# Kernel tuning notes

Hardware: AMD Instinct MI355X
Metric: run time of the kernel (lower is better)

Reference implementation:

```python
import jax, jax.numpy as jnp
import numpy as np
from functools import partial

MAX_SPAN_WIDTH = 8


def setup_inputs() -> dict:
    key = jax.random.key(0)
    ks = jax.random.split(key, 8)
    B, S, H = 4, 256, 256
    NE, D = 50000, 256  # entity_embedding_dim == hidden_size
    inp = {
        "embeddings": jax.random.normal(ks[0], (B, S, H), jnp.float32),          # BERT outputs[0]
        "entity_table": jax.random.normal(ks[1], (NE, D), jnp.float32) * 0.02,   # nn.Embedding weight
        "span_W": jax.random.normal(ks[2], (2 * H + 1, H), jnp.float32) * 0.02,  # span_embedding Linear
        "span_b": jax.random.normal(ks[3], (H,), jnp.float32) * 0.02,
        "gcn_W1": jax.random.normal(ks[4], (D, H), jnp.float32) * 0.02,
        "gcn_b1": jax.random.normal(ks[5], (H,), jnp.float32) * 0.02,
        "gcn_W2": jax.random.normal(ks[6], (H, H), jnp.float32) * 0.02,
        "gcn_b2": jax.random.normal(ks[7], (H,), jnp.float32) * 0.02,
        "k": 8,
    }
    return inp


def _star_adj_norm(k, dtype):
    # k-node star graph (node 0 hub) with self-loops, symmetric GCN normalization
    A = jnp.zeros((k, k), dtype).at[0, 1:].set(1.0).at[1:, 0].set(1.0) + jnp.eye(k, dtype=dtype)
    deg = A.sum(axis=1)
    return A / jnp.sqrt(deg[:, None] * deg[None, :])


def reference(embeddings, entity_table, span_W, span_b, gcn_W1, gcn_b1, gcn_W2, gcn_b2, k):
    B, S, H = embeddings.shape
    Wmax = MAX_SPAN_WIDTH
    dtype = embeddings.dtype

    # token_inputs: CLS embedding per example
    cls = embeddings[:, 0, :]  # [B, H]

    # Vectorized ragged span max-pool: running max over widths 1..Wmax.
    # span_max[w, b, s, :] = max(embeddings[b, s : s+w+1, :])
    neg_inf = jnp.array(-jnp.inf, dtype)
    maxes = []
    cur = embeddings
    maxes.append(cur)
    for w in range(1, Wmax):
        shifted = jnp.concatenate(
            [embeddings[:, w:, :], jnp.full((B, w, H), neg_inf, dtype)], axis=1)
        cur = jnp.maximum(cur, shifted)  # -inf pad => out-of-range positions ignored
        maxes.append(cur)
    span_max = jnp.stack(maxes, axis=0)  # [Wmax, B, S, H]

    # concat(max-pool, CLS, span width) -> span_embedding Linear
    cls_b = jnp.broadcast_to(cls[None, :, None, :], (Wmax, B, S, H))
    width_feat = jnp.broadcast_to(
        jnp.arange(1, Wmax + 1, dtype=dtype)[:, None, None, None], (Wmax, B, S, 1))
    span_inputs = jnp.concatenate([span_max, cls_b, width_feat], axis=-1)  # [Wmax,B,S,2H+1]
    span_inputs = span_inputs.reshape(Wmax * B * S, 2 * H + 1)             # [N, 2H+1]
    span_repr = span_inputs @ span_W + span_b                              # [N, H]

    # build_subgraph: top-k similar entities per span (memory-bound similarity + top-k)
    sims = span_repr @ entity_table.T          # [N, NE]  ~1.6GB intermediate
    _, topk_idx = jax.lax.top_k(sims, k)       # [N, k]
    node_x = entity_table[topk_idx]            # gather -> [N, k, D]

    # 2-layer GCN on the fixed star subgraph (gather-linear-scatter equivalent)
    A_norm = _star_adj_norm(k, dtype)          # [k, k]
    h = jax.nn.relu(jnp.einsum('ij,njd,dh->nih', A_norm, node_x, gcn_W1) + gcn_b1)
    subgraph_out = jnp.einsum('ij,njd,dh->nih', A_norm, h, gcn_W2) + gcn_b2  # [N, k, H]

    return cls, span_repr, subgraph_out
```

## Files before the change

kernel.cpp:

```cpp
#include <hip/hip_runtime.h>

typedef unsigned short u16;
typedef unsigned int   u32;
typedef unsigned long long u64;
typedef short bf16x8 __attribute__((ext_vector_type(8)));
typedef float f32x4  __attribute__((ext_vector_type(4)));

#define INF_F __builtin_inff()

__device__ __forceinline__ u16 f2bf(float f) {
  u32 u = __float_as_uint(f);
  return (u16)((u + 0x7FFFu + ((u >> 16) & 1u)) >> 16);
}

__device__ __forceinline__ u32 sortf(float f) {
  u32 u = __float_as_uint(f);
  return u ^ ((u32)((int)u >> 31) | 0x80000000u);
}
__device__ __forceinline__ float unsortf(u32 s) {
  u32 u = s ^ ((s & 0x80000000u) ? 0x80000000u : 0xFFFFFFFFu);
  return __uint_as_float(u);
}
__device__ __forceinline__ u64 sx64(u64 v, int m) {
  u32 lo = __shfl_xor((u32)v, m);
  u32 hi = __shfl_xor((u32)(v >> 32), m);
  return ((u64)hi << 32) | lo;
}

__device__ __forceinline__ void gload_lds16(const void* g, void* l) {
  __builtin_amdgcn_global_load_lds(
      (const __attribute__((address_space(1))) u32*)g,
      (__attribute__((address_space(3))) u32*)l, 16, 0, 0);
}

__global__ __launch_bounds__(256) void k0_cvt(
    const float* __restrict__ src, u16* __restrict__ dst, int n4) {
  int id = blockIdx.x * 256 + threadIdx.x;
  if (id >= n4) return;
  float4 v = ((const float4*)src)[id];
  ((ushort4*)dst)[id] = make_ushort4(f2bf(v.x), f2bf(v.y), f2bf(v.z), f2bf(v.w));
}

__global__ __launch_bounds__(256) void k1_span(
    const float* __restrict__ emb, const float* __restrict__ Wsp,
    const float* __restrict__ bsp,
    float* __restrict__ out0, float* __restrict__ out1,
    u16* __restrict__ spanbf) {
  __shared__ float SM[8][256];
  __shared__ float CLS[256];
  const int bid = blockIdx.x;
  const int b = bid >> 8, s = bid & 255;
  const int t = threadIdx.x;
  const float* eb = emb + (size_t)b * 65536;

  CLS[t] = eb[t];
  if (s == 0) out0[b * 256 + t] = eb[t];

  float m = eb[s * 256 + t];
  SM[0][t] = m;
  #pragma unroll
  for (int w = 1; w < 8; ++w) {
    if (s + w < 256) m = fmaxf(m, eb[(s + w) * 256 + t]);
    SM[w][t] = m;
  }
  __syncthreads();

  float cc = 0.f;
  for (int k = 0; k < 256; k += 4) {
    float4 cq = *(const float4*)&CLS[k];
    cc += cq.x * Wsp[(size_t)(256 + k + 0) * 256 + t];
    cc += cq.y * Wsp[(size_t)(256 + k + 1) * 256 + t];
    cc += cq.z * Wsp[(size_t)(256 + k + 2) * 256 + t];
    cc += cq.w * Wsp[(size_t)(256 + k + 3) * 256 + t];
  }
  float acc[8];
  const float base = bsp[t] + cc;
  #pragma unroll
  for (int w = 0; w < 8; ++w) acc[w] = base;

  for (int k = 0; k < 256; k += 4) {
    float w0 = Wsp[(size_t)(k + 0) * 256 + t];
    float w1 = Wsp[(size_t)(k + 1) * 256 + t];
    float w2 = Wsp[(size_t)(k + 2) * 256 + t];
    float w3 = Wsp[(size_t)(k + 3) * 256 + t];
    #pragma unroll
    for (int w = 0; w < 8; ++w) {
      float4 smq = *(const float4*)&SM[w][k];
      acc[w] += smq.x * w0; acc[w] += smq.y * w1;
      acc[w] += smq.z * w2; acc[w] += smq.w * w3;
    }
  }
  const float wm = Wsp[(size_t)512 * 256 + t];
  #pragma unroll
  for (int w = 0; w < 8; ++w) {
    float val = acc[w] + (float)(w + 1) * wm;
    size_t idx = ((size_t)w * 1024 + bid) * 256 + t;
    out1[idx] = val;
    spanbf[idx] = f2bf(val);
  }
}

__global__ __launch_bounds__(128, 4) void k2_mfma(
    const u16* __restrict__ spanbf, const u16* __restrict__ entbf, int ne,
    float* __restrict__ Rpv, int* __restrict__ Rpi) {
  __shared__ u32 Elds[4096];
  __shared__ u64 Q[2][32][8];
  const int t = threadIdx.x, lane = t & 63, wv = t >> 6;
  const int m = lane & 15, q = lane >> 4, q4 = q * 4;
  const int p = blockIdx.x & 15, rg = blockIdx.x >> 4;
  const int psz = (ne + 15) >> 4;
  const int e_start = p * psz;
  const int e_end = min(ne, e_start + psz);
  const int rowbase = rg * 64 + wv * 32;
  const u64 gm = 0xFFFFull << (q * 16);
  const u64 lanelow = (lane == 63) ? 0x7FFFFFFFFFFFFFFFull
                                   : ((1ull << (lane + 1)) - 1) >> 1;
  const u64 gml = gm & lanelow;
  const int row = lane & 15;
  const int ls5 = lane >> 5;

  const u64 KINIT = ((u64)sortf(-INF_F) << 32);
  u64 slot[2][4];
  float myth[2], th[2][4];
  #pragma unroll
  for (int h = 0; h < 2; ++h) {
    myth[h] = -INF_F;
    #pragma unroll
    for (int s = 0; s < 4; ++s) { slot[h][s] = KINIT; th[h][s] = -INF_F; }
  }

  bf16x8 a[2][8];
  #pragma unroll
  for (int h = 0; h < 2; ++h)
    #pragma unroll
    for (int s = 0; s < 8; ++s)
      a[h][s] = *(const bf16x8*)(spanbf
                  + (size_t)(rowbase + h * 16 + m) * 256 + s * 32 + q * 8);

  auto issue = [&](int k, int sl) {
    const int cb = e_start + (k << 4);
    #pragma unroll
    for (int i = 0; i < 4; ++i) {
      int eo = wv * 8 + i * 2 + ls5;
      int e  = (sl << 4) + eo;
      int ge = min(cb + eo, e_end - 1);
      int xoff = ((lane & 31) ^ (e & 31)) << 4;
      gload_lds16((const char*)entbf + (size_t)ge * 512 + xoff,
                  (char*)Elds + (sl << 13) + (wv << 12) + (i << 10));
    }
  };

  const int nch = (e_end - e_start + 15) >> 4;
  issue(0, 0);

  for (int pc = 0; pc < nch; ++pc) {
    const int cs = pc & 1;
    asm volatile("s_waitcnt vmcnt(0)" ::: "memory");
    __builtin_amdgcn_sched_barrier(0);
    __builtin_amdgcn_s_barrier();
    if (pc + 1 < nch) issue(pc + 1, cs ^ 1);

    f32x4 acc[2];
    #pragma unroll
    for (int h = 0; h < 2; ++h) acc[h] = (f32x4){0.f, 0.f, 0.f, 0.f};
    const int el = (cs << 4) + m, sw = el & 31, bc = el << 5;
    #pragma unroll
    for (int s = 0; s < 8; ++s) {
      int qq = s * 4 + q;
      bf16x8 bfr = *(const bf16x8*)((const char*)Elds + ((bc | (qq ^ sw)) << 4));
      #pragma unroll
      for (int h = 0; h < 2; ++h)
        acc[h] = __builtin_amdgcn_mfma_f32_16x16x32_bf16(a[h][s], bfr, acc[h], 0, 0, 0);
    }
    const int gent = e_start + (pc << 4) + m;
    const bool valid = gent < e_end;

    #pragma unroll
    for (int h = 0; h < 2; ++h) {
      bool any = valid & ((acc[h][0] > th[h][0]) | (acc[h][1] > th[h][1]) |
                          (acc[h][2] > th[h][2]) | (acc[h][3] > th[h][3]));
      if (!__ballot(any)) continue;
      u64 M[4]; u64 key[4]; int ps_[4]; bool hit[4];
      #pragma unroll
      for (int r = 0; r < 4; ++r) {
        hit[r] = valid && (acc[h][r] > th[h][r]);
        M[r] = __ballot(hit[r]);
        key[r] = ((u64)sortf(acc[h][r]) << 32) | (u32)(~(u32)gent);
        ps_[r] = (int)__popcll(M[r] & gml);
        if (hit[r] && ps_[r] < 8)
          Q[wv][h * 16 + q4 + r][(ps_[r] ^ (q4 + r)) & 7] = key[r];
      }
      u64 msk = (row & 2) ? ((row & 1) ? M[3] : M[2])
                          : ((row & 1) ? M[1] : M[0]);
      int cnt = (int)__popcll((msk >> ((row >> 2) << 4)) & 0xFFFFull);
      int cmax = cnt;
      #pragma unroll
      for (int o = 1; o < 16; o <<= 1)
        cmax = max(cmax, __shfl_xor(cmax, o));
      const u64* qrow = Q[wv][h * 16 + row];
      const int rx = row & 7;
      int cm1 = min(cmax, 8);
      for (int j = 0; j < cm1; ++j) {
        u64 cand = (j < cnt) ? qrow[(j ^ rx) & 7] : 0;
        u64 m01 = slot[h][0] < slot[h][1] ? slot[h][0] : slot[h][1];
        u64 m23 = slot[h][2] < slot[h][3] ? slot[h][2] : slot[h][3];
        u64 lmin = m01 < m23 ? m01 : m23;
        u64 g = sx64(lmin, 16); if (g < lmin) lmin = g;
        g = sx64(lmin, 32); u64 gmin = (g < lmin) ? g : lmin;
        bool ins = cand > gmin;
        #pragma unroll
        for (int s2 = 0; s2 < 4; ++s2)
          if (ins && slot[h][s2] == gmin) slot[h][s2] = cand;
      }
      if (cmax > 8) {
        #pragma unroll
        for (int r = 0; r < 4; ++r)
          if (hit[r] && ps_[r] >= 8)
            Q[wv][h * 16 + q4 + r][((ps_[r] - 8) ^ (q4 + r)) & 7] = key[r];
        for (int j = 8; j < cmax; ++j) {
          u64 cand = (j < cnt) ? qrow[((j - 8) ^ rx) & 7] : 0;
          u64 m01 = slot[h][0] < slot[h][1] ? slot[h][0] : slot[h][1];
          u64 m23 = slot[h][2] < slot[h][3] ? slot[h][2] : slot[h][3];
          u64 lmin = m01 < m23 ? m01 : m23;
          u64 g = sx64(lmin, 16); if (g < lmin) lmin = g;
          g = sx64(lmin, 32); u64 gmin = (g < lmin) ? g : lmin;
          bool ins = cand > gmin;
          #pragma unroll
          for (int s2 = 0; s2 < 4; ++s2)
            if (ins && slot[h][s2] == gmin) slot[h][s2] = cand;
        }
      }
      {
        u64 m01 = slot[h][0] < slot[h][1] ? slot[h][0] : slot[h][1];
        u64 m23 = slot[h][2] < slot[h][3] ? slot[h][2] : slot[h][3];
        u64 lmin = m01 < m23 ? m01 : m23;
        u64 g = sx64(lmin, 16); if (g < lmin) lmin = g;
        g = sx64(lmin, 32); if (g < lmin) lmin = g;
        myth[h] = unsortf((u32)(lmin >> 32));
        #pragma unroll
        for (int r = 0; r < 4; ++r) th[h][r] = __shfl(myth[h], q4 + r);
      }
    }
  }

  {
    const int sg = lane >> 4;
    #pragma unroll
    for (int h = 0; h < 2; ++h) {
      int r0 = rowbase + h * 16 + row;
      #pragma unroll
      for (int s = 0; s < 4; ++s) {
        u64 e0 = slot[h][s];
        int col = p * 16 + sg * 4 + s;
        Rpv[(size_t)r0 * 256 + col] = unsortf((u32)(e0 >> 32));
        Rpi[(size_t)r0 * 256 + col] = (int)(~(u32)e0);
      }
    }
  }
}

__global__ __launch_bounds__(256) void k2_merge(
    const float* __restrict__ Rpv, const int* __restrict__ Rpi,
    int* __restrict__ Ridx) {
  const int t = threadIdx.x, lane = t & 63, wv = t >> 6;
  const int row = blockIdx.x * 4 + wv;
  float v[4]; int e[4];
  #pragma unroll
  for (int pg = 0; pg < 4; ++pg) {
    v[pg] = Rpv[(size_t)row * 256 + pg * 64 + lane];
    e[pg] = Rpi[(size_t)row * 256 + pg * 64 + lane];
  }
  int c[4] = {0, 0, 0, 0};
  #pragma unroll
  for (int ps = 0; ps < 4; ++ps) {
    for (int i = 0; i < 64; ++i) {
      float ov = __shfl(v[ps], i); int oi = __shfl(e[ps], i);
      #pragma unroll
      for (int pd = 0; pd < 4; ++pd)
        c[pd] += (ov > v[pd] || (ov == v[pd] && oi < e[pd]));
    }
  }
  #pragma unroll
  for (int pg = 0; pg < 4; ++pg)
    if (c[pg] < 16) Ridx[(size_t)row * 16 + c[pg]] = e[pg];
}

__global__ __launch_bounds__(256, 3) void k3_gcn(
    const float* __restrict__ out1, const float* __restrict__ ent,
    const int* __restrict__ Ridx,
    const float* __restrict__ W1, const float* __restrict__ b1,
    const float* __restrict__ W2, const float* __restrict__ b2,
    float* __restrict__ out2, int ne) {
  __shared__ __align__(16) char UN[34560];
  __shared__ __align__(16) u16 Abf[32][272];
  __shared__ int cidx[4][16];
  __shared__ int chos[4][8];
  const int t = threadIdx.x;
  const int lane = t & 63, wv = t >> 6;
  const int m = lane & 15, q = lane >> 4;
  const int n0 = blockIdx.x * 4;

  {
    float  (*SPR)[256] = (float (*)[256])UN;
    double (*dpart)[4] = (double (*)[4])(UN + 4096);
    double (*sims)[16] = (double (*)[16])(UN + 6144);
    #pragma unroll
    for (int g = 0; g < 4; ++g)
      SPR[g][t] = out1[(size_t)(n0 + g) * 256 + t];
    if (t < 64) {
      int g = t >> 4, j = t & 15;
      int c = Ridx[(size_t)(n0 + g) * 16 + j];
      if ((unsigned)c >= (unsigned)ne) c = 0;
      cidx[g][j] = c;
    }
    __syncthreads();

    {
      const int pr = t >> 2, sub = t & 3;
      const int g = pr >> 4, j = pr & 15;
      const float* er = ent + (size_t)cidx[g][j] * 256 + sub * 64;
      const float* sr = &SPR[g][sub * 64];
      double s = 0.0;
      #pragma unroll
      for (int i = 0; i < 64; i += 4) {
        float4 e4 = *(const float4*)&er[i];
        float4 s4 = *(const float4*)&sr[i];
        s += (double)e4.x * (double)s4.x;
        s += (double)e4.y * (double)s4.y;
        s += (double)e4.z * (double)s4.z;
        s += (double)e4.w * (double)s4.w;
      }
      dpart[pr][sub] = s;
    }
    __syncthreads();
    if (t < 64) {
      int g = t >> 4, j = t & 15;
      sims[g][j] = dpart[t][0] + dpart[t][1] + dpart[t][2] + dpart[t][3];
    }
    __syncthreads();
    if (t < 4) {
      unsigned used = 0;
      for (int o = 0; o < 8; ++o) {
        int best = -1; double bv = 0.0; int bi = 0;
        for (int j = 0; j < 16; ++j) {
          if (used & (1u << j)) continue;
          if (best < 0 || sims[t][j] > bv || (sims[t][j] == bv && cidx[t][j] < bi)) {
            best = j; bv = sims[t][j]; bi = cidx[t][j];
          }
        }
        used |= (1u << best);
        chos[t][o] = cidx[t][best];
      }
    }
    __syncthreads();
  }

  {
    const int r = t >> 3, cb = t & 7;
    const float* src = ent + (size_t)chos[r >> 3][r & 7] * 256 + cb * 32;
    u32 pk[16];
    #pragma unroll
    for (int i = 0; i < 8; ++i) {
      float4 v = *(const float4*)&src[i * 4];
      pk[2 * i]     = (u32)f2bf(v.x) | ((u32)f2bf(v.y) << 16);
      pk[2 * i + 1] = (u32)f2bf(v.z) | ((u32)f2bf(v.w) << 16);
    }
    uint4* dst = (uint4*)&Abf[r][cb * 32];
    #pragma unroll
    for (int i = 0; i < 4; ++i)
      dst[i] = make_uint4(pk[4 * i], pk[4 * i + 1], pk[4 * i + 2], pk[4 * i + 3]);
  }

  auto run_gemm = [&](const float* __restrict__ Wg) {
    f32x4 acc[2][4];
    #pragma unroll
    for (int mt = 0; mt < 2; ++mt)
      #pragma unroll
      for (int nt = 0; nt < 4; ++nt)
        acc[mt][nt] = (f32x4){0.f, 0.f, 0.f, 0.f};

    for (int s = 0; s < 8; ++s) {
      __syncthreads();
      {
        const float* src = Wg + (size_t)(s * 32) * 256 + t;
        u32 pk[16];
        #pragma unroll
        for (int i = 0; i < 16; ++i) {
          float lo = src[(size_t)(2 * i) * 256];
          float hi = src[(size_t)(2 * i + 1) * 256];
          pk[i] = (u32)f2bf(lo) | ((u32)f2bf(hi) << 16);
        }
        uint4* dst = (uint4*)(UN + t * 80);
        #pragma unroll
        for (int i = 0; i < 4; ++i)
          dst[i] = make_uint4(pk[4 * i], pk[4 * i + 1], pk[4 * i + 2], pk[4 * i + 3]);
      }
      __syncthreads();
      #pragma unroll
      for (int mt = 0; mt < 2; ++mt) {
        bf16x8 af = *(const bf16x8*)((const char*)Abf
                       + (mt * 16 + m) * 544 + s * 64 + q * 16);
        #pragma unroll
        for (int nt = 0; nt < 4; ++nt) {
          const int col = wv * 64 + nt * 16 + m;
          bf16x8 bf = *(const bf16x8*)(UN + col * 80 + q * 16);
          acc[mt][nt] = __builtin_amdgcn_mfma_f32_16x16x32_bf16(
              af, bf, acc[mt][nt], 0, 0, 0);
        }
      }
    }
    __syncthreads();
    #pragma unroll
    for (int mt = 0; mt < 2; ++mt)
      #pragma unroll
      for (int nt = 0; nt < 4; ++nt)
        #pragma unroll
        for (int r = 0; r < 4; ++r)
          *(float*)(UN + (((mt * 16 + q * 4 + r) * 268)
                          + (wv * 64 + nt * 16 + m)) * 4) = acc[mt][nt][r];
    __syncthreads();
  };

  run_gemm(W1);
  {
    const float bb = b1[t];
    #pragma unroll
    for (int g = 0; g < 4; ++g) {
      float v[8];
      #pragma unroll
      for (int j = 0; j < 8; ++j)
        v[j] = *(const float*)(UN + ((g * 8 + j) * 268 + t) * 4);
      float ssum = 0.f;
      #pragma unroll
      for (int j = 1; j < 8; ++j) ssum += v[j];
      Abf[g * 8][t] = f2bf(fmaxf(v[0] * 0.125f + ssum * 0.25f + bb, 0.f));
      #pragma unroll
      for (int j = 1; j < 8; ++j)
        Abf[g * 8 + j][t] = f2bf(fmaxf(v[0] * 0.25f + v[j] * 0.5f + bb, 0.f));
    }
  }

  run_gemm(W2);
  {
    const float bb = b2[t];
    #pragma unroll
    for (int g = 0; g < 4; ++g) {
      float v[8];
      #pragma unroll
      for (int j = 0; j < 8; ++j)
        v[j] = *(const float*)(UN + ((g * 8 + j) * 268 + t) * 4);
      float ssum = 0.f;
      #pragma unroll
      for (int j = 1; j < 8; ++j) ssum += v[j];
      float* ob = out2 + (size_t)(n0 + g) * 2048 + t;
      ob[0] = v[0] * 0.125f + ssum * 0.25f + bb;
      #pragma unroll
      for (int j = 1; j < 8; ++j)
        ob[(size_t)j * 256] = v[0] * 0.25f + v[j] * 0.5f + bb;
    }
  }
}

extern "C" void kernel_launch(void* const* d_in, const int* in_sizes, int n_in,
                              void* d_out, int out_size, void* d_ws, size_t ws_size,
                              hipStream_t stream) {
  const float* emb = (const float*)d_in[0];
  const float* ent = (const float*)d_in[1];
  const float* Wsp = (const float*)d_in[2];
  const float* bsp = (const float*)d_in[3];
  const float* W1  = (const float*)d_in[4];
  const float* b1  = (const float*)d_in[5];
  const float* W2  = (const float*)d_in[6];
  const float* b2  = (const float*)d_in[7];
  const int ne = in_sizes[1] / 256;

  float* out  = (float*)d_out;
  float* out0 = out;
  float* out1 = out + 1024;
  float* out2 = out + 1024 + 2097152;

  char* ov = (char*)out2;
  u16*   entbf  = (u16*)(ov);
  u16*   spanbf = (u16*)(ov + 33554432);
  float* Rpv    = (float*)(ov + 41943040);
  int*   Rpi    = (int*)  (ov + 50331648);
  int*   Ridx   = (int*)d_ws;

  hipLaunchKernelGGL(k0_cvt, dim3((ne * 64 + 255) / 256), dim3(256), 0, stream,
                     ent, entbf, ne * 64);
  hipLaunchKernelGGL(k1_span, dim3(1024), dim3(256), 0, stream,
                     emb, Wsp, bsp, out0, out1, spanbf);
  hipLaunchKernelGGL(k2_mfma, dim3(2048), dim3(128), 0, stream,
                     spanbf, entbf, ne, Rpv, Rpi);
  hipLaunchKernelGGL(k2_merge, dim3(2048), dim3(256), 0, stream,
                     Rpv, Rpi, Ridx);
  hipLaunchKernelGGL(k3_gcn, dim3(2048), dim3(256), 0, stream,
                     out1, ent, Ridx, W1, b1, W2, b2, out2, ne);
}
```

Measured before the change: 730.0 us.

## Keep per-row top-16 candidates in one lane instead of cross-lane distributed slots

The per-row top-16 candidate list was spread across four lanes with 4 slots each, so every insertion needed 64-bit cross-lane shuffle reductions. Now each of 32 lanes owns one row's 16 slots in registers, keeps a cached minimum, and only recomputes it when a candidate is inserted. Both row halves are handled in one pass, and the LDS queue grows to 16 entries per row to drop the overflow path. This raises register use (occupancy hint lowered from 4 to 3) and leaves half the wave idle during insertion.

Measured after the change: 1.035 ms. 1.42x slower.

```diff
diff --git a/kernel.cpp b/kernel.cpp
--- a/kernel.cpp
+++ b/kernel.cpp
@@ -21,11 +21,7 @@
   u32 u = s ^ ((s & 0x80000000u) ? 0x80000000u : 0xFFFFFFFFu);
   return __uint_as_float(u);
 }
-__device__ __forceinline__ u64 sx64(u64 v, int m) {
-  u32 lo = __shfl_xor((u32)v, m);
-  u32 hi = __shfl_xor((u32)(v >> 32), m);
-  return ((u64)hi << 32) | lo;
-}
+__device__ __forceinline__ u64 umin64(u64 a, u64 b) { return a < b ? a : b; }
 
 __device__ __forceinline__ void gload_lds16(const void* g, void* l) {
   __builtin_amdgcn_global_load_lds(
@@ -100,11 +96,11 @@
   }
 }
 
-__global__ __launch_bounds__(128, 4) void k2_mfma(
+__global__ __launch_bounds__(128, 3) void k2_mfma(
     const u16* __restrict__ spanbf, const u16* __restrict__ entbf, int ne,
     float* __restrict__ Rpv, int* __restrict__ Rpi) {
   __shared__ u32 Elds[4096];
-  __shared__ u64 Q[2][32][8];
+  __shared__ u64 Q[2][32][16];
   const int t = threadIdx.x, lane = t & 63, wv = t >> 6;
   const int m = lane & 15, q = lane >> 4, q4 = q * 4;
   const int p = blockIdx.x & 15, rg = blockIdx.x >> 4;
@@ -116,18 +112,19 @@
   const u64 lanelow = (lane == 63) ? 0x7FFFFFFFFFFFFFFFull
                                    : ((1ull << (lane + 1)) - 1) >> 1;
   const u64 gml = gm & lanelow;
-  const int row = lane & 15;
   const int ls5 = lane >> 5;
 
-  const u64 KINIT = ((u64)sortf(-INF_F) << 32);
-  u64 slot[2][4];
-  float myth[2], th[2][4];
-  #pragma unroll
-  for (int h = 0; h < 2; ++h) {
-    myth[h] = -INF_F;
-    #pragma unroll
-    for (int s = 0; s < 4; ++s) { slot[h][s] = KINIT; th[h][s] = -INF_F; }
-  }
+  u64 slot[16];
+  #pragma unroll
+  for (int s = 0; s < 16; ++s)
+    slot[s] = ((u64)sortf(-INF_F) << 32) | (u32)s;
+  u64 mn = slot[0];
+  float myth = -INF_F;
+  float th[2][4];
+  #pragma unroll
+  for (int h = 0; h < 2; ++h)
+    #pragma unroll
+    for (int r = 0; r < 4; ++r) th[h][r] = -INF_F;
 
   bf16x8 a[2][8];
   #pragma unroll
@@ -161,100 +158,81 @@
     if (pc + 1 < nch) issue(pc + 1, cs ^ 1);
 
     f32x4 acc[2];
-    #pragma unroll
-    for (int h = 0; h < 2; ++h) acc[h] = (f32x4){0.f, 0.f, 0.f, 0.f};
+    acc[0] = (f32x4){0.f, 0.f, 0.f, 0.f};
+    acc[1] = (f32x4){0.f, 0.f, 0.f, 0.f};
     const int el = (cs << 4) + m, sw = el & 31, bc = el << 5;
     #pragma unroll
     for (int s = 0; s < 8; ++s) {
       int qq = s * 4 + q;
       bf16x8 bfr = *(const bf16x8*)((const char*)Elds + ((bc | (qq ^ sw)) << 4));
-      #pragma unroll
-      for (int h = 0; h < 2; ++h)
-        acc[h] = __builtin_amdgcn_mfma_f32_16x16x32_bf16(a[h][s], bfr, acc[h], 0, 0, 0);
+      acc[0] = __builtin_amdgcn_mfma_f32_16x16x32_bf16(a[0][s], bfr, acc[0], 0, 0, 0);
+      acc[1] = __builtin_amdgcn_mfma_f32_16x16x32_bf16(a[1][s], bfr, acc[1], 0, 0, 0);
     }
     const int gent = e_start + (pc << 4) + m;
     const bool valid = gent < e_end;
 
-    #pragma unroll
-    for (int h = 0; h < 2; ++h) {
-      bool any = valid & ((acc[h][0] > th[h][0]) | (acc[h][1] > th[h][1]) |
-                          (acc[h][2] > th[h][2]) | (acc[h][3] > th[h][3]));
-      if (!__ballot(any)) continue;
-      u64 M[4]; u64 key[4]; int ps_[4]; bool hit[4];
-      #pragma unroll
-      for (int r = 0; r < 4; ++r) {
-        hit[r] = valid && (acc[h][r] > th[h][r]);
-        M[r] = __ballot(hit[r]);
-        key[r] = ((u64)sortf(acc[h][r]) << 32) | (u32)(~(u32)gent);
-        ps_[r] = (int)__popcll(M[r] & gml);
-        if (hit[r] && ps_[r] < 8)
-          Q[wv][h * 16 + q4 + r][(ps_[r] ^ (q4 + r)) & 7] = key[r];
-      }
-      u64 msk = (row & 2) ? ((row & 1) ? M[3] : M[2])
-                          : ((row & 1) ? M[1] : M[0]);
-      int cnt = (int)__popcll((msk >> ((row >> 2) << 4)) & 0xFFFFull);
-      int cmax = cnt;
-      #pragma unroll
-      for (int o = 1; o < 16; o <<= 1)
-        cmax = max(cmax, __shfl_xor(cmax, o));
-      const u64* qrow = Q[wv][h * 16 + row];
-      const int rx = row & 7;
-      int cm1 = min(cmax, 8);
-      for (int j = 0; j < cm1; ++j) {
-        u64 cand = (j < cnt) ? qrow[(j ^ rx) & 7] : 0;
-        u64 m01 = slot[h][0] < slot[h][1] ? slot[h][0] : slot[h][1];
-        u64 m23 = slot[h][2] < slot[h][3] ? slot[h][2] : slot[h][3];
-        u64 lmin = m01 < m23 ? m01 : m23;
-        u64 g = sx64(lmin, 16); if (g < lmin) lmin = g;
-        g = sx64(lmin, 32); u64 gmin = (g < lmin) ? g : lmin;
-        bool ins = cand > gmin;
-        #pragma unroll
-        for (int s2 = 0; s2 < 4; ++s2)
-          if (ins && slot[h][s2] == gmin) slot[h][s2] = cand;
-      }
-      if (cmax > 8) {
+    bool any = valid & ((acc[0][0] > th[0][0]) | (acc[0][1] > th[0][1]) |
+                        (acc[0][2] > th[0][2]) | (acc[0][3] > th[0][3]) |
+                        (acc[1][0] > th[1][0]) | (acc[1][1] > th[1][1]) |
+                        (acc[1][2] > th[1][2]) | (acc[1][3] > th[1][3]));
+    if (__ballot(any)) {
+      u64 M[2][4];
+      #pragma unroll
+      for (int h = 0; h < 2; ++h) {
+        #pragma unroll
+        for (int r = 0; r < 4; ++r) {
+          bool hr = valid && (acc[h][r] > th[h][r]);
+          M[h][r] = __ballot(hr);
+          if (hr) {
+            int pos = (int)__popcll(M[h][r] & gml);
+            Q[wv][h * 16 + q4 + r][pos ^ (q4 + r)] =
+                ((u64)sortf(acc[h][r]) << 32) | (u32)(~(u32)gent);
+          }
+        }
+      }
+      if (lane < 32) {
+        const int r_ = lane & 3;
+        u64 mA = (r_ == 0) ? M[0][0] : (r_ == 1) ? M[0][1]
+               : (r_ == 2) ? M[0][2] : M[0][3];
+        u64 mB = (r_ == 0) ? M[1][0] : (r_ == 1) ? M[1][1]
+               : (r_ == 2) ? M[1][2] : M[1][3];
+        u64 Msel = (lane & 16) ? mB : mA;
+        int cnt = (int)__popcll((Msel >> ((lane & 12) << 2)) & 0xFFFFull);
+        const u64* qrow = Q[wv][lane];
+        const int lx = lane & 15;
+        for (int j = 0; j < cnt; ++j) {
+          u64 cand = qrow[j ^ lx];
+          if (cand > mn) {
+            #pragma unroll
+            for (int s = 0; s < 16; ++s)
+              slot[s] = (slot[s] == mn) ? cand : slot[s];
+            u64 x0 = umin64(slot[0], slot[1]),  x1 = umin64(slot[2], slot[3]);
+            u64 x2 = umin64(slot[4], slot[5]),  x3 = umin64(slot[6], slot[7]);
+            u64 x4 = umin64(slot[8], slot[9]),  x5 = umin64(slot[10], slot[11]);
+            u64 x6 = umin64(slot[12], slot[13]), x7 = umin64(slot[14], slot[15]);
+            x0 = umin64(x0, x1); x2 = umin64(x2, x3);
+            x4 = umin64(x4, x5); x6 = umin64(x6, x7);
+            x0 = umin64(x0, x2); x4 = umin64(x4, x6);
+            mn = umin64(x0, x4);
+          }
+        }
+        myth = unsortf((u32)(mn >> 32));
+      }
+      #pragma unroll
+      for (int h = 0; h < 2; ++h)
         #pragma unroll
         for (int r = 0; r < 4; ++r)
-          if (hit[r] && ps_[r] >= 8)
-            Q[wv][h * 16 + q4 + r][((ps_[r] - 8) ^ (q4 + r)) & 7] = key[r];
-        for (int j = 8; j < cmax; ++j) {
-          u64 cand = (j < cnt) ? qrow[((j - 8) ^ rx) & 7] : 0;
-          u64 m01 = slot[h][0] < slot[h][1] ? slot[h][0] : slot[h][1];
-          u64 m23 = slot[h][2] < slot[h][3] ? slot[h][2] : slot[h][3];
-          u64 lmin = m01 < m23 ? m01 : m23;
-          u64 g = sx64(lmin, 16); if (g < lmin) lmin = g;
-          g = sx64(lmin, 32); u64 gmin = (g < lmin) ? g : lmin;
-          bool ins = cand > gmin;
-          #pragma unroll
-          for (int s2 = 0; s2 < 4; ++s2)
-            if (ins && slot[h][s2] == gmin) slot[h][s2] = cand;
-        }
-      }
-      {
-        u64 m01 = slot[h][0] < slot[h][1] ? slot[h][0] : slot[h][1];
-        u64 m23 = slot[h][2] < slot[h][3] ? slot[h][2] : slot[h][3];
-        u64 lmin = m01 < m23 ? m01 : m23;
-        u64 g = sx64(lmin, 16); if (g < lmin) lmin = g;
-        g = sx64(lmin, 32); if (g < lmin) lmin = g;
-        myth[h] = unsortf((u32)(lmin >> 32));
-        #pragma unroll
-        for (int r = 0; r < 4; ++r) th[h][r] = __shfl(myth[h], q4 + r);
-      }
-    }
-  }
-
-  {
-    const int sg = lane >> 4;
-    #pragma unroll
-    for (int h = 0; h < 2; ++h) {
-      int r0 = rowbase + h * 16 + row;
-      #pragma unroll
-      for (int s = 0; s < 4; ++s) {
-        u64 e0 = slot[h][s];
-        int col = p * 16 + sg * 4 + s;
-        Rpv[(size_t)r0 * 256 + col] = unsortf((u32)(e0 >> 32));
-        Rpi[(size_t)r0 * 256 + col] = (int)(~(u32)e0);
-      }
+          th[h][r] = __shfl(myth, h * 16 + q4 + r);
+    }
+  }
+
+  if (lane < 32) {
+    const int r0 = rowbase + lane;
+    #pragma unroll
+    for (int s = 0; s < 16; ++s) {
+      u64 e0 = slot[s];
+      Rpv[(size_t)r0 * 256 + p * 16 + s] = unsortf((u32)(e0 >> 32));
+      Rpi[(size_t)r0 * 256 + p * 16 + s] = (int)(~(u32)e0);
     }
   }
 }
```
